# Kernel tuning notes

Measured on AMD Instinct MI355X. Metric: run time of the kernel, lower is better.

Reference implementation:

```python
import jax, jax.numpy as jnp
import numpy as np

NUM_LAYERS = 4
CODEBOOK_SIZE = 2048
DIM = 256
N = 32768
BETA = 0.25
EPS = 1e-12  # F.normalize eps


def setup_inputs() -> dict:
    key = jax.random.key(0)
    kx, kc = jax.random.split(key)
    x = jax.random.normal(kx, (N, DIM), dtype=jnp.float32)
    # nn.Embedding default init: N(0, 1)
    codebooks = jax.random.normal(kc, (NUM_LAYERS, CODEBOOK_SIZE, DIM), dtype=jnp.float32)
    return {"x": x, "codebooks": codebooks}


def reference(x, codebooks):
    sg = jax.lax.stop_gradient
    residual = x
    all_indices = []
    decoded = jnp.zeros_like(x)
    total_loss = jnp.zeros((), dtype=x.dtype)
    n_elem = x.size
    for layer in range(NUM_LAYERS):
        cb = codebooks[layer]                      # [K, D] (raw, used for gather)
        norm = jnp.linalg.norm(cb, axis=-1, keepdims=True)
        cbn = cb / jnp.maximum(norm, EPS)          # L2-normalized, used for distances
        # squared L2 distances; argmin is invariant to the sqrt in torch.cdist
        d2 = (
            jnp.sum(residual * residual, axis=-1, keepdims=True)
            - 2.0 * residual @ cbn.T
            + jnp.sum(cbn * cbn, axis=-1)
        )                                          # [N, K]
        idx = jnp.argmin(d2, axis=-1)              # [N]
        all_indices.append(idx)
        q = cb[idx]                                # [N, D] gather from RAW codebook
        codebook_loss = jnp.sum((residual - sg(q)) ** 2) / n_elem
        commitment_loss = jnp.sum((sg(residual) - q) ** 2) / n_elem
        total_loss = total_loss + codebook_loss + BETA * commitment_loss
        decoded = decoded + q
        # residual = residual - (residual + sg(q - residual)) == sg(residual - q)
        residual = sg(residual - q)
    stru_ids = jnp.stack(all_indices, axis=1)      # [N, L]
    return stru_ids, decoded, total_loss
```

## Files before the change

### kernel.cpp

```cpp
#include <hip/hip_runtime.h>
#include <math.h>

#define L_NUM 4
#define K_CB  2048
#define D_DIM 256
#define N_ROWS 32768
#define CAP 56
#define WACC  0.12f
#define WACC2 0.125f

typedef _Float16 half8 __attribute__((ext_vector_type(8)));
typedef _Float16 half4v __attribute__((ext_vector_type(4)));
typedef float f32x16 __attribute__((ext_vector_type(16)));

__device__ __forceinline__ void gl_lds16(const void* g, void* l) {
  __builtin_amdgcn_global_load_lds(
      (const __attribute__((address_space(1))) void*)g,
      (__attribute__((address_space(3))) void*)l, 16, 0, 0);
}
__device__ __forceinline__ unsigned fenc(float f) {
  unsigned u = __float_as_uint(f);
  return (u & 0x80000000u) ? ~u : (u | 0x80000000u);
}
__device__ __forceinline__ float fdec(unsigned k) {
  unsigned u = (k & 0x80000000u) ? (k ^ 0x80000000u) : ~k;
  return __uint_as_float(u);
}

__device__ __forceinline__ float tmax64(const f32x16& a, const f32x16& b,
                                        const f32x16& c, const f32x16& d) {
  float m[16];
  #pragma unroll
  for (int i = 0; i < 16; ++i)
    m[i] = fmaxf(fmaxf(a[i], b[i]), fmaxf(c[i], d[i]));
  #pragma unroll
  for (int s2 = 8; s2 >= 1; s2 >>= 1)
    #pragma unroll
    for (int i = 0; i < s2; ++i) m[i] = fmaxf(m[i], m[i + s2]);
  return m[0];
}

__global__ __launch_bounds__(64)
void prep_all_kernel(const float* __restrict__ cb,
                     float* __restrict__ cbn,
                     double* __restrict__ c2d,
                     _Float16* __restrict__ cb16) {
  const int b = blockIdx.x;
  const int k = b & 2047, l = b >> 11;
  const int lane = threadIdx.x;
  float4 v = reinterpret_cast<const float4*>(cb + (size_t)b * D_DIM)[lane];
  float s = v.x*v.x + v.y*v.y + v.z*v.z + v.w*v.w;
  #pragma unroll
  for (int m = 1; m < 64; m <<= 1) s += __shfl_xor(s, m, 64);
  const float den = fmaxf(sqrtf(s), 1e-12f);
  v.x /= den; v.y /= den; v.z /= den; v.w /= den;
  reinterpret_cast<float4*>(cbn + (size_t)b * D_DIM)[lane] = v;
  double td = (double)v.x*v.x + (double)v.y*v.y + (double)v.z*v.z + (double)v.w*v.w;
  #pragma unroll
  for (int m = 1; m < 64; m <<= 1) td += __shfl_xor(td, m, 64);
  if (lane == 0) c2d[b] = td;
  half4v h;
  h[0] = (_Float16)v.x; h[1] = (_Float16)v.y; h[2] = (_Float16)v.z; h[3] = (_Float16)v.w;
  const int tile = k >> 9, col = k & 511;
  const int kchunk = lane >> 3;
  const int sslot  = (lane >> 1) & 3;
  const int rem    = (lane & 1) * 4;
  const size_t off = (size_t)l * (K_CB * D_DIM)
                   + (size_t)(tile * 8 + kchunk) * 16384
                   + (size_t)sslot * 4096 + (size_t)col * 8 + rem;
  *(half4v*)(cb16 + off) = h;
}

__global__ __launch_bounds__(512, 2)
void rq_fused_kernel(const float* __restrict__ x,
                     const float* __restrict__ cb,
                     const float* __restrict__ cbn,
                     const double* __restrict__ c2d,
                     const _Float16* __restrict__ cb16,
                     float* __restrict__ out_ids,
                     float* __restrict__ out_dec,
                     double* __restrict__ dloss) {
  extern __shared__ char sm[];
  _Float16* A16   = (_Float16*)sm;
  _Float16* Bs    = (_Float16*)(sm + 65536);
  unsigned* cp    = (unsigned*)(sm + 131072);
  int*      cn    = (int*)(sm + 131072 + 128*CAP*4);
  unsigned* gmax  = (unsigned*)((char*)cn + 512);
  unsigned* bestp = (unsigned*)((char*)gmax + 512);

  const int t = threadIdx.x;
  const int wid = t >> 6, ln = t & 63;
  const int l31 = ln & 31, hl = ln >> 5;
  const int rowg = wid >> 2, colg = wid & 3;
  const int urow = t >> 2, qo = (t & 3) * 64;
  const int row0 = blockIdx.x * 128;
  const int mrow0 = rowg * 64 + l31, mrow1 = mrow0 + 32;

  float r[64];
  {
    const float4* xg = (const float4*)(x + (size_t)(row0 + urow) * D_DIM + qo);
    #pragma unroll
    for (int i = 0; i < 16; ++i) {
      const float4 a = xg[i];
      r[i*4+0]=a.x; r[i*4+1]=a.y; r[i*4+2]=a.z; r[i*4+3]=a.w;
    }
  }
  #pragma unroll
  for (int j = 0; j < 8; ++j) {
    half8 h;
    #pragma unroll
    for (int e = 0; e < 8; ++e) h[e] = (_Float16)r[j*8+e];
    const int slot = (t & 3) * 8 + j;
    *(half8*)(A16 + slot*1024 + urow*8) = h;
  }
  if (t < 128) { cn[t] = 0; gmax[t] = 0u; bestp[t] = 0u; }
  int id0 = 0, id1 = 0, id2 = 0, id3 = 0;
  double lloss = 0.0;

  {
    const char* B0 = (const char*)cb16;
    #pragma unroll
    for (int i = 0; i < 4; ++i)
      gl_lds16(B0 + t*16 + i*8192, (char*)Bs + t*16 + i*8192);
  }

  #pragma unroll 1
  for (int l = 0; l < L_NUM; ++l) {
    const char* Bimg = (const char*)cb16 + (size_t)l * (K_CB * D_DIM * 2);
    __syncthreads();

    f32x16 acc[4][2];

    #pragma unroll 1
    for (int g = 0; g < 32; ++g) {
      __builtin_amdgcn_s_barrier();
      __builtin_amdgcn_sched_barrier(0);
      if (g < 31) {
        char* dst = (char*)Bs + ((g + 1) & 1) * 32768;
        const char* src = Bimg + (size_t)(g + 1) * 32768;
        #pragma unroll
        for (int i = 0; i < 4; ++i)
          gl_lds16(src + t*16 + i*8192, dst + t*16 + i*8192);
        asm volatile("s_waitcnt vmcnt(4)" ::: "memory");
      } else {
        asm volatile("s_waitcnt vmcnt(0)" ::: "memory");
      }
      __builtin_amdgcn_s_barrier();

      if ((g & 7) == 0) {
        #pragma unroll
        for (int bi = 0; bi < 4; ++bi)
          #pragma unroll
          for (int ai = 0; ai < 2; ++ai)
            #pragma unroll
            for (int e = 0; e < 16; ++e) acc[bi][ai][e] = 0.f;
      }
      const _Float16* Bb = Bs + (g & 1) * 16384;
      const int cK = g & 7;
      #pragma unroll
      for (int ks2 = 0; ks2 < 2; ++ks2) {
        const int sa = cK*4 + ks2*2 + hl;
        const int sb = ks2*2 + hl;
        half8 af[2], bf[4];
        af[0] = *(const half8*)(A16 + sa*1024 + mrow0*8);
        af[1] = *(const half8*)(A16 + sa*1024 + mrow1*8);
        #pragma unroll
        for (int bi = 0; bi < 4; ++bi) {
          const int col = colg*128 + bi*32 + l31;
          bf[bi] = *(const half8*)(Bb + sb*4096 + col*8);
        }
        #pragma unroll
        for (int bi = 0; bi < 4; ++bi) {
          acc[bi][0] = __builtin_amdgcn_mfma_f32_32x32x16_f16(bf[bi], af[0], acc[bi][0], 0, 0, 0);
          acc[bi][1] = __builtin_amdgcn_mfma_f32_32x32x16_f16(bf[bi], af[1], acc[bi][1], 0, 0, 0);
        }
      }
      if ((g & 7) == 7) {
        const int ct = g >> 3;
        #pragma unroll
        for (int ai = 0; ai < 2; ++ai) {
          const int mrow = ai ? mrow1 : mrow0;
          const float m = ai ? tmax64(acc[0][1], acc[1][1], acc[2][1], acc[3][1])
                             : tmax64(acc[0][0], acc[1][0], acc[2][0], acc[3][0]);
          atomicMax(&gmax[mrow], fenc(m));
          const float thr = fdec(gmax[mrow]) - WACC;
          #pragma unroll
          for (int bi = 0; bi < 4; ++bi)
            #pragma unroll
            for (int rg = 0; rg < 16; ++rg) {
              const float v = acc[bi][ai][rg];
              if (v >= thr) {
                const unsigned q = (unsigned)((v + 64.f) * 16384.f);
                const unsigned cidx = (unsigned)(ct*512 + colg*128 + bi*32
                                                 + 4*hl + (rg & 3) + 8*(rg >> 2));
                const unsigned pk = (q << 11) | cidx;
                atomicMax(&bestp[mrow], pk);
                const int slot = atomicAdd(&cn[mrow], 1);
                if (slot < CAP) cp[mrow*CAP + slot] = pk;
              }
            }
        }
      }
    }
    __syncthreads();

    if (l < 3) {
      const char* Bn = (const char*)cb16 + (size_t)(l + 1) * (K_CB * D_DIM * 2);
      #pragma unroll
      for (int i = 0; i < 4; ++i)
        gl_lds16(Bn + t*16 + i*8192, (char*)Bs + t*16 + i*8192);
    }

    {
      const float thr2 = fdec(gmax[urow]) - WACC2;
      const int m = min(cn[urow], CAP);
      double bsc = (double)INFINITY; int bidx = 0x7fffffff;
      #pragma unroll 1
      for (int j = 0; j <= m; ++j) {
        const unsigned p = (j < m) ? cp[urow*CAP + j] : bestp[urow];
        const float v = (float)(p >> 11) * (1.f/16384.f) - 64.f;
        if (j < m && v < thr2) continue;
        const int cidx = (int)(p & 2047u);
        const float4* cpn = (const float4*)(cbn + ((size_t)l*K_CB + cidx)*D_DIM + qo);
        double s = 0.0;
        #pragma unroll
        for (int i = 0; i < 16; ++i) {
          const float4 a = cpn[i];
          s = fma((double)r[i*4+0], (double)a.x, s);
          s = fma((double)r[i*4+1], (double)a.y, s);
          s = fma((double)r[i*4+2], (double)a.z, s);
          s = fma((double)r[i*4+3], (double)a.w, s);
        }
        s += __shfl_xor(s, 1, 64);
        s += __shfl_xor(s, 2, 64);
        const double sc = -2.0 * s + c2d[l*K_CB + cidx];
        if (sc < bsc || (sc == bsc && cidx < bidx)) { bsc = sc; bidx = cidx; }
      }
      bidx &= 2047;
      if (l == 0) id0 = bidx; else if (l == 1) id1 = bidx;
      else if (l == 2) id2 = bidx; else id3 = bidx;
      if ((t & 3) == 0) out_ids[(size_t)(row0 + urow)*L_NUM + l] = (float)bidx;

      const float4* qg = (const float4*)(cb + ((size_t)l*K_CB + bidx)*D_DIM + qo);
      #pragma unroll
      for (int i = 0; i < 16; ++i) {
        const float4 q = qg[i];
        r[i*4+0] -= q.x; r[i*4+1] -= q.y; r[i*4+2] -= q.z; r[i*4+3] -= q.w;
        lloss += (double)r[i*4+0]*r[i*4+0] + (double)r[i*4+1]*r[i*4+1]
               + (double)r[i*4+2]*r[i*4+2] + (double)r[i*4+3]*r[i*4+3];
      }
      if (l < 3) {
        #pragma unroll
        for (int j = 0; j < 8; ++j) {
          half8 h;
          #pragma unroll
          for (int e = 0; e < 8; ++e) h[e] = (_Float16)r[j*8+e];
          const int slot = (t & 3) * 8 + j;
          *(half8*)(A16 + slot*1024 + urow*8) = h;
        }
      }
    }
    __syncthreads();
    if (l < 3 && t < 128) { cn[t] = 0; gmax[t] = 0u; bestp[t] = 0u; }
  }

  {
    float dec[64];
    #pragma unroll
    for (int l2 = 0; l2 < L_NUM; ++l2) {
      const int idl = (l2 == 0) ? id0 : (l2 == 1) ? id1 : (l2 == 2) ? id2 : id3;
      const float4* qg = (const float4*)(cb + ((size_t)l2*K_CB + idl)*D_DIM + qo);
      #pragma unroll
      for (int i = 0; i < 16; ++i) {
        const float4 q = qg[i];
        if (l2 == 0) { dec[i*4+0]=q.x; dec[i*4+1]=q.y; dec[i*4+2]=q.z; dec[i*4+3]=q.w; }
        else { dec[i*4+0]+=q.x; dec[i*4+1]+=q.y; dec[i*4+2]+=q.z; dec[i*4+3]+=q.w; }
      }
    }
    float4* dg = (float4*)(out_dec + (size_t)(row0 + urow)*D_DIM + qo);
    #pragma unroll
    for (int i = 0; i < 16; ++i)
      dg[i] = make_float4(dec[i*4+0], dec[i*4+1], dec[i*4+2], dec[i*4+3]);
  }

  double* lw = (double*)cp;
  #pragma unroll
  for (int m = 1; m < 64; m <<= 1) lloss += __shfl_xor(lloss, m, 64);
  if (ln == 0) lw[wid] = lloss;
  __syncthreads();
  if (t == 0) {
    double s2 = 0.0;
    #pragma unroll
    for (int j = 0; j < 8; ++j) s2 += lw[j];
    atomicAdd(dloss, s2);
  }
}

__global__ void rq_fin_kernel(const double* __restrict__ dls, float* __restrict__ out_loss) {
  out_loss[0] = (float)(dls[0] * 1.25 / 8388608.0);
}

extern "C" void kernel_launch(void* const* d_in, const int* in_sizes, int n_in,
                              void* d_out, int out_size, void* d_ws, size_t ws_size,
                              hipStream_t stream) {
  const float* x  = (const float*)d_in[0];
  const float* cb = (const float*)d_in[1];
  float* out      = (float*)d_out;
  float* out_ids  = out;
  float* out_dec  = out + (size_t)N_ROWS * L_NUM;
  float* out_loss = out_dec + (size_t)N_ROWS * D_DIM;

  char* w = (char*)d_ws;
  double* dls = (double*)w;                   w += 256;
  double* c2d = (double*)w;                   w += (size_t)L_NUM*K_CB*8;
  float* cbn = (float*)w;                     w += (size_t)L_NUM*K_CB*D_DIM*4;
  _Float16* cb16 = (_Float16*)w;              w += (size_t)L_NUM*K_CB*D_DIM*2;

  hipMemsetAsync(dls, 0, sizeof(double), stream);
  prep_all_kernel<<<L_NUM*K_CB, 64, 0, stream>>>(cb, cbn, c2d, cb16);

  const size_t smem = 65536 + 65536 + 128*CAP*4 + 512 + 512 + 512;
  hipFuncSetAttribute(reinterpret_cast<const void*>(rq_fused_kernel),
                      hipFuncAttributeMaxDynamicSharedMemorySize, (int)smem);
  rq_fused_kernel<<<N_ROWS/128, 512, smem, stream>>>(x, cb, cbn, c2d, cb16,
                                                     out_ids, out_dec, dls);
  rq_fin_kernel<<<1, 1, 0, stream>>>(dls, out_loss);
}
```

Measured before the change: 354.9 us.

## Switch codebook staging to triple-buffered 16KB chunks with two-ahead prefetch

Halves the per-stage B chunk from 32KB to 16KB (one k-step of 32) and rotates three LDS buffers so loads run two stages ahead instead of one. The prep kernel's fp16 codebook layout is changed to match the smaller chunk. Shrinking the B staging area from 64KB to 48KB cuts shared memory per block, and s_setprio is raised around the MFMA burst. The cost is twice as many barrier-separated iterations per layer with less compute between barriers.

```diff
diff --git a/kernel.cpp b/kernel.cpp
--- a/kernel.cpp
+++ b/kernel.cpp
@@ -61,12 +61,12 @@
   if (lane == 0) c2d[b] = td;
   half4v h;
   h[0] = (_Float16)v.x; h[1] = (_Float16)v.y; h[2] = (_Float16)v.z; h[3] = (_Float16)v.w;
-  const int tile = k >> 9, col = k & 511;
-  const int kchunk = lane >> 3;
-  const int sslot  = (lane >> 1) & 3;
+  const int ct = k >> 9, col = k & 511;
+  const int kchunk = lane >> 2;
+  const int sslot  = (lane >> 1) & 1;
   const int rem    = (lane & 1) * 4;
   const size_t off = (size_t)l * (K_CB * D_DIM)
-                   + (size_t)(tile * 8 + kchunk) * 16384
+                   + (size_t)(ct * 16 + kchunk) * 8192
                    + (size_t)sslot * 4096 + (size_t)col * 8 + rem;
   *(half4v*)(cb16 + off) = h;
 }
@@ -83,8 +83,8 @@
   extern __shared__ char sm[];
   _Float16* A16   = (_Float16*)sm;
   _Float16* Bs    = (_Float16*)(sm + 65536);
-  unsigned* cp    = (unsigned*)(sm + 131072);
-  int*      cn    = (int*)(sm + 131072 + 128*CAP*4);
+  unsigned* cp    = (unsigned*)(sm + 65536 + 49152);
+  int*      cn    = (int*)((char*)cp + 128*CAP*4);
   unsigned* gmax  = (unsigned*)((char*)cn + 512);
   unsigned* bestp = (unsigned*)((char*)gmax + 512);
 
@@ -119,9 +119,10 @@
 
   {
     const char* B0 = (const char*)cb16;
-    #pragma unroll
-    for (int i = 0; i < 4; ++i)
-      gl_lds16(B0 + t*16 + i*8192, (char*)Bs + t*16 + i*8192);
+    gl_lds16(B0 + t*16,         (char*)Bs + t*16);
+    gl_lds16(B0 + t*16 + 8192,  (char*)Bs + t*16 + 8192);
+    gl_lds16(B0 + 16384 + t*16,        (char*)Bs + 16384 + t*16);
+    gl_lds16(B0 + 16384 + t*16 + 8192, (char*)Bs + 16384 + t*16 + 8192);
   }
 
   #pragma unroll 1
@@ -130,24 +131,27 @@
     __syncthreads();
 
     f32x16 acc[4][2];
+    int cur = 0;
 
     #pragma unroll 1
-    for (int g = 0; g < 32; ++g) {
+    for (int g = 0; g < 64; ++g) {
       __builtin_amdgcn_s_barrier();
       __builtin_amdgcn_sched_barrier(0);
-      if (g < 31) {
-        char* dst = (char*)Bs + ((g + 1) & 1) * 32768;
-        const char* src = Bimg + (size_t)(g + 1) * 32768;
-        #pragma unroll
-        for (int i = 0; i < 4; ++i)
-          gl_lds16(src + t*16 + i*8192, dst + t*16 + i*8192);
+      if (g < 62) {
+        const int tgt = (cur == 0) ? 2 : cur - 1;
+        const char* src = Bimg + (size_t)(g + 2) * 16384;
+        char* dst = (char*)Bs + tgt * 16384;
+        gl_lds16(src + t*16,        dst + t*16);
+        gl_lds16(src + t*16 + 8192, dst + t*16 + 8192);
         asm volatile("s_waitcnt vmcnt(4)" ::: "memory");
+      } else if (g == 62) {
+        asm volatile("s_waitcnt vmcnt(2)" ::: "memory");
       } else {
         asm volatile("s_waitcnt vmcnt(0)" ::: "memory");
       }
       __builtin_amdgcn_s_barrier();
 
-      if ((g & 7) == 0) {
+      if ((g & 15) == 0) {
         #pragma unroll
         for (int bi = 0; bi < 4; ++bi)
           #pragma unroll
@@ -155,28 +159,26 @@
             #pragma unroll
             for (int e = 0; e < 16; ++e) acc[bi][ai][e] = 0.f;
       }
-      const _Float16* Bb = Bs + (g & 1) * 16384;
-      const int cK = g & 7;
+      const _Float16* Bb = Bs + cur * 8192;
+      const int sa = ((g & 15) << 1) + hl;
+      half8 af[2], bf[4];
+      af[0] = *(const half8*)(A16 + sa*1024 + mrow0*8);
+      af[1] = *(const half8*)(A16 + sa*1024 + mrow1*8);
       #pragma unroll
-      for (int ks2 = 0; ks2 < 2; ++ks2) {
-        const int sa = cK*4 + ks2*2 + hl;
-        const int sb = ks2*2 + hl;
-        half8 af[2], bf[4];
-        af[0] = *(const half8*)(A16 + sa*1024 + mrow0*8);
-        af[1] = *(const half8*)(A16 + sa*1024 + mrow1*8);
-        #pragma unroll
-        for (int bi = 0; bi < 4; ++bi) {
-          const int col = colg*128 + bi*32 + l31;
-          bf[bi] = *(const half8*)(Bb + sb*4096 + col*8);
-        }
-        #pragma unroll
-        for (int bi = 0; bi < 4; ++bi) {
-          acc[bi][0] = __builtin_amdgcn_mfma_f32_32x32x16_f16(bf[bi], af[0], acc[bi][0], 0, 0, 0);
-          acc[bi][1] = __builtin_amdgcn_mfma_f32_32x32x16_f16(bf[bi], af[1], acc[bi][1], 0, 0, 0);
-        }
-      }
-      if ((g & 7) == 7) {
-        const int ct = g >> 3;
+      for (int bi = 0; bi < 4; ++bi) {
+        const int col = colg*128 + bi*32 + l31;
+        bf[bi] = *(const half8*)(Bb + hl*4096 + col*8);
+      }
+      __builtin_amdgcn_s_setprio(1);
+      #pragma unroll
+      for (int bi = 0; bi < 4; ++bi) {
+        acc[bi][0] = __builtin_amdgcn_mfma_f32_32x32x16_f16(bf[bi], af[0], acc[bi][0], 0, 0, 0);
+        acc[bi][1] = __builtin_amdgcn_mfma_f32_32x32x16_f16(bf[bi], af[1], acc[bi][1], 0, 0, 0);
+      }
+      __builtin_amdgcn_s_setprio(0);
+
+      if ((g & 15) == 15) {
+        const int ct = g >> 4;
         #pragma unroll
         for (int ai = 0; ai < 2; ++ai) {
           const int mrow = ai ? mrow1 : mrow0;
@@ -201,14 +203,16 @@
             }
         }
       }
+      cur = (cur == 2) ? 0 : cur + 1;
     }
     __syncthreads();
 
     if (l < 3) {
       const char* Bn = (const char*)cb16 + (size_t)(l + 1) * (K_CB * D_DIM * 2);
-      #pragma unroll
-      for (int i = 0; i < 4; ++i)
-        gl_lds16(Bn + t*16 + i*8192, (char*)Bs + t*16 + i*8192);
+      gl_lds16(Bn + t*16,         (char*)Bs + t*16);
+      gl_lds16(Bn + t*16 + 8192,  (char*)Bs + t*16 + 8192);
+      gl_lds16(Bn + 16384 + t*16,        (char*)Bs + 16384 + t*16);
+      gl_lds16(Bn + 16384 + t*16 + 8192, (char*)Bs + 16384 + t*16 + 8192);
     }
 
     {
@@ -319,7 +323,7 @@
   hipMemsetAsync(dls, 0, sizeof(double), stream);
   prep_all_kernel<<<L_NUM*K_CB, 64, 0, stream>>>(cb, cbn, c2d, cb16);
 
-  const size_t smem = 65536 + 65536 + 128*CAP*4 + 512 + 512 + 512;
+  const size_t smem = 65536 + 49152 + 128*CAP*4 + 512 + 512 + 512;
   hipFuncSetAttribute(reinterpret_cast<const void*>(rq_fused_kernel),
                       hipFuncAttributeMaxDynamicSharedMemorySize, (int)smem);
   rq_fused_kernel<<<N_ROWS/128, 512, smem, stream>>>(x, cb, cbn, c2d, cb16,
```

Measured after the change: 369.4 us. 1.04x slower.
